# Kernel tuning notes

Measured on AMD Instinct MI355X. Metric: run time of the kernel, lower is better.

The kernel has to match this reference:

```python
import jax, jax.numpy as jnp
import numpy as np

S, B, C = 7, 2, 20
EPS = 1e-6
LAMBDA_COORD = 5.0
LAMBDA_NOOBJ = 0.5


def setup_inputs() -> dict:
    key = jax.random.key(0)
    k1, k2 = jax.random.split(key)
    N = 16384
    p = jax.random.uniform(k1, (N, S, S, B * 5 + C), dtype=jnp.float32)
    a = jax.random.uniform(k2, (N, S, S, B * 5 + C), dtype=jnp.float32)
    return {"p": p, "a": a}


def _attr(t, i):
    # i-th attribute of each of the B boxes: channels C+i, C+i+5, ... -> [N,S,S,B]
    return t[..., C + i::5]


def _coords(t):
    x, y, w, h = _attr(t, 0), _attr(t, 1), _attr(t, 2), _attr(t, 3)
    tl = jnp.stack((x - w / 2.0, y - h / 2.0), axis=-1)  # [N,S,S,B,2]
    br = jnp.stack((x + w / 2.0, y + h / 2.0), axis=-1)
    return tl, br


def _sse(x, y):
    return jnp.sum((x - y) ** 2)


def reference(p, a):
    # pairwise IoU between predicted boxes (axis 3) and target boxes (axis 4)
    p_tl, p_br = _coords(p)
    a_tl, a_br = _coords(a)
    tl = jnp.maximum(p_tl[:, :, :, :, None, :], a_tl[:, :, :, None, :, :])  # [N,S,S,B,B,2]
    br = jnp.minimum(p_br[:, :, :, :, None, :], a_br[:, :, :, None, :, :])
    sides = jnp.clip(br - tl, 0.0)
    inter = sides[..., 0] * sides[..., 1]  # [N,S,S,B,B]
    p_area = (_attr(p, 2) * _attr(p, 3))[:, :, :, :, None]
    a_area = (_attr(a, 2) * _attr(a, 3))[:, :, :, None, :]
    union = p_area + a_area - inter
    zero_union = union == 0.0
    iou = jnp.where(zero_union, 0.0, inter) / jnp.where(zero_union, EPS, union)
    max_iou = jnp.max(iou, axis=-1)  # [N,S,S,B]

    obj_i = (_attr(a, 4) > 0.0)[..., 0:1]  # [N,S,S,1]
    responsible = jnp.argmax(max_iou, axis=-1, keepdims=True) == jnp.arange(B)  # [N,S,S,B]
    obj_ij = (obj_i & responsible).astype(p.dtype)
    noobj_ij = 1.0 - obj_ij

    loss_x = _sse(obj_ij * _attr(a, 0), obj_ij * _attr(p, 0))
    loss_y = _sse(obj_ij * _attr(a, 1), obj_ij * _attr(p, 1))
    loss_w = _sse(obj_ij * jnp.sign(_attr(a, 2)) * jnp.sqrt(_attr(a, 2) + EPS),
                  obj_ij * jnp.sign(_attr(p, 2)) * jnp.sqrt(_attr(p, 2) + EPS))
    loss_h = _sse(obj_ij * jnp.sign(_attr(a, 3)) * jnp.sqrt(_attr(a, 3) + EPS),
                  obj_ij * jnp.sign(_attr(p, 3)) * jnp.sqrt(_attr(p, 3) + EPS))
    loss_conf_obj = _sse(obj_ij * obj_ij, obj_ij * _attr(p, 4))
    loss_conf_noobj = _sse(noobj_ij * obj_ij, noobj_ij * _attr(p, 4))
    obj_if = obj_i.astype(p.dtype)
    cls_loss = _sse(obj_if * p[..., 5 * B:], obj_if * a[..., 5 * B:])

    return (LAMBDA_COORD * (loss_x + loss_y + loss_w + loss_h)
            + loss_conf_obj + LAMBDA_NOOBJ * loss_conf_noobj + cls_loss)
```

## Files before the change

### kernel.cpp

```cpp
#include <hip/hip_runtime.h>


#define CH    30
#define EPSL  1e-6f
#define TPB   256

__device__ __forceinline__ float sgnf(float x) {
    return (x > 0.0f) ? 1.0f : ((x < 0.0f) ? -1.0f : 0.0f);
}

__global__ __launch_bounds__(TPB) void yolo_loss_kernel(const float* __restrict__ p,
                                                        const float* __restrict__ a,
                                                        float* __restrict__ out,
                                                        long long n_cells) {
    __shared__ float wsum[TPB / 64];

    const int tid = threadIdx.x;
    const long long cell = (long long)blockIdx.x * TPB + tid;

    float lsum = 0.0f;
    if (cell < n_cells) {
        const float2* cp2 = (const float2*)(p + cell * CH + 10);
        const float2* ca2 = (const float2*)(a + cell * CH + 10);
        float pd[20], ad[20];
#pragma unroll
        for (int i = 0; i < 10; ++i) {
            const float2 v = cp2[i];
            pd[2 * i] = v.x; pd[2 * i + 1] = v.y;
        }
#pragma unroll
        for (int i = 0; i < 10; ++i) {
            const float2 v = ca2[i];
            ad[2 * i] = v.x; ad[2 * i + 1] = v.y;
        }

        float pxv[2], pyv[2], pwv[2], phv[2], pcv[2];
        float axv[2], ayv[2], awv[2], ahv[2];
#pragma unroll
        for (int b = 0; b < 2; ++b) {
            pxv[b] = pd[10 + 5 * b]; pyv[b] = pd[11 + 5 * b];
            pwv[b] = pd[12 + 5 * b]; phv[b] = pd[13 + 5 * b];
            pcv[b] = pd[14 + 5 * b];
            axv[b] = ad[10 + 5 * b]; ayv[b] = ad[11 + 5 * b];
            awv[b] = ad[12 + 5 * b]; ahv[b] = ad[13 + 5 * b];
        }
        const bool obj = ad[14] > 0.0f;

        float miou[2];
#pragma unroll
        for (int pb = 0; pb < 2; ++pb) {
            const float p_tlx = pxv[pb] - 0.5f * pwv[pb];
            const float p_tly = pyv[pb] - 0.5f * phv[pb];
            const float p_brx = pxv[pb] + 0.5f * pwv[pb];
            const float p_bry = pyv[pb] + 0.5f * phv[pb];
            const float p_area = pwv[pb] * phv[pb];
            float best = -3.4e38f;
#pragma unroll
            for (int ab = 0; ab < 2; ++ab) {
                const float a_tlx = axv[ab] - 0.5f * awv[ab];
                const float a_tly = ayv[ab] - 0.5f * ahv[ab];
                const float a_brx = axv[ab] + 0.5f * awv[ab];
                const float a_bry = ayv[ab] + 0.5f * ahv[ab];
                float sx = fminf(p_brx, a_brx) - fmaxf(p_tlx, a_tlx);
                float sy = fminf(p_bry, a_bry) - fmaxf(p_tly, a_tly);
                sx = fmaxf(sx, 0.0f);
                sy = fmaxf(sy, 0.0f);
                const float inter = sx * sy;
                const float uni = p_area + awv[ab] * ahv[ab] - inter;
                const float iou = (uni == 0.0f) ? 0.0f : (inter / uni);
                best = fmaxf(best, iou);
            }
            miou[pb] = best;
        }
        const int resp = (miou[1] > miou[0]) ? 1 : 0;

#pragma unroll
        for (int b = 0; b < 2; ++b) {
            const bool oij = obj && (b == resp);
            if (oij) {
                const float dx = axv[b] - pxv[b];
                const float dy = ayv[b] - pyv[b];
                const float dw = sgnf(awv[b]) * sqrtf(awv[b] + EPSL) - sgnf(pwv[b]) * sqrtf(pwv[b] + EPSL);
                const float dh = sgnf(ahv[b]) * sqrtf(ahv[b] + EPSL) - sgnf(phv[b]) * sqrtf(phv[b] + EPSL);
                const float dc = 1.0f - pcv[b];
                lsum += 5.0f * (dx * dx + dy * dy + dw * dw + dh * dh) + dc * dc;
            } else {
                lsum += 0.5f * pcv[b] * pcv[b];
            }
        }

        if (obj) {
#pragma unroll
            for (int k = 0; k < 20; ++k) {
                const float d = pd[k] - ad[k];
                lsum += d * d;
            }
        }
    }

    float v = lsum;
#pragma unroll
    for (int off = 32; off > 0; off >>= 1)
        v += __shfl_down(v, off, 64);
    if ((tid & 63) == 0) wsum[tid >> 6] = v;
    __syncthreads();
    if (tid == 0) {
        float t = 0.0f;
#pragma unroll
        for (int w = 0; w < TPB / 64; ++w) t += wsum[w];
        atomicAdd(out, t);
    }
}

extern "C" void kernel_launch(void* const* d_in, const int* in_sizes, int n_in,
                              void* d_out, int out_size, void* d_ws, size_t ws_size,
                              hipStream_t stream) {
    const float* p = (const float*)d_in[0];
    const float* a = (const float*)d_in[1];
    float* out = (float*)d_out;

    const long long n_cells = (long long)in_sizes[0] / CH;
    const int grid = (int)((n_cells + TPB - 1) / TPB);

    hipMemsetAsync(d_out, 0, sizeof(float), stream);
    yolo_loss_kernel<<<grid, TPB, 0, stream>>>(p, a, out, n_cells);
}
```

Baseline: 204.0 us.

## Coalesce global loads via per-wave LDS transpose staging

Each wave now loads its 64 cells' relevant 20 floats cooperatively as float2 with lane-contiguous addresses, then transposes them through a padded shared-memory tile so each lane gets its own cell's data. This targets the strided per-thread 120-byte-stride loads of the old version, which gave poorly coalesced memory accesses. It adds LDS traffic and several block-wide barriers, and sets a minimum-occupancy launch bound that may constrain registers.

```diff
diff --git a/kernel.cpp b/kernel.cpp
--- a/kernel.cpp
+++ b/kernel.cpp
@@ -1,39 +1,82 @@
 #include <hip/hip_runtime.h>
 
 
-#define CH    30
-#define EPSL  1e-6f
-#define TPB   256
+#define CH       30
+#define EPSL     1e-6f
+#define TPB      256
+#define WAVES    (TPB / 64)
+#define CSTRIDE  22
+#define WTILE    (64 * CSTRIDE)
 
 __device__ __forceinline__ float sgnf(float x) {
     return (x > 0.0f) ? 1.0f : ((x < 0.0f) ? -1.0f : 0.0f);
 }
 
-__global__ __launch_bounds__(TPB) void yolo_loss_kernel(const float* __restrict__ p,
-                                                        const float* __restrict__ a,
-                                                        float* __restrict__ out,
-                                                        long long n_cells) {
-    __shared__ float wsum[TPB / 64];
+__global__ __launch_bounds__(TPB, 6) void yolo_loss_kernel(const float* __restrict__ p,
+                                                           const float* __restrict__ a,
+                                                           float* __restrict__ out,
+                                                           long long n_cells) {
+    __shared__ __align__(16) float sbuf[WAVES * WTILE];
+    __shared__ float wsum[WAVES];
 
-    const int tid = threadIdx.x;
-    const long long cell = (long long)blockIdx.x * TPB + tid;
+    const int tid  = threadIdx.x;
+    const int wave = tid >> 6;
+    const int lane = tid & 63;
+
+    const long long wave_cell0 = (long long)blockIdx.x * TPB + wave * 64;
+    int nc_wave = (int)min((long long)64, n_cells - wave_cell0);
+    if (nc_wave < 0) nc_wave = 0;
+
+    const char* pb = (const char*)p + wave_cell0 * 120LL;
+    const char* ab = (const char*)a + wave_cell0 * 120LL;
+    float* wbuf = &sbuf[wave * WTILE];
+
+    float2 rp[10], ra[10];
+    int cc[10], ss[10];
+#pragma unroll
+    for (int k = 0; k < 10; ++k) {
+        const int i = lane + 64 * k;
+        const int c = i / 10;
+        const int s = i - 10 * c;
+        cc[k] = c; ss[k] = s;
+        const int off = c * 120 + 40 + 8 * s;
+        if (c < nc_wave) rp[k] = *(const float2*)(pb + off);
+    }
+#pragma unroll
+    for (int k = 0; k < 10; ++k) {
+        const int off = cc[k] * 120 + 40 + 8 * ss[k];
+        if (cc[k] < nc_wave) ra[k] = *(const float2*)(ab + off);
+    }
+
+#pragma unroll
+    for (int k = 0; k < 10; ++k)
+        if (cc[k] < nc_wave)
+            *(float2*)&wbuf[cc[k] * CSTRIDE + 2 * ss[k]] = rp[k];
+    __syncthreads();
+
+    float pd[20];
+#pragma unroll
+    for (int s = 0; s < 10; ++s) {
+        const float2 v = *(const float2*)&wbuf[lane * CSTRIDE + 2 * s];
+        pd[2 * s] = v.x; pd[2 * s + 1] = v.y;
+    }
+    __syncthreads();
+
+#pragma unroll
+    for (int k = 0; k < 10; ++k)
+        if (cc[k] < nc_wave)
+            *(float2*)&wbuf[cc[k] * CSTRIDE + 2 * ss[k]] = ra[k];
+    __syncthreads();
+
+    float ad[20];
+#pragma unroll
+    for (int s = 0; s < 10; ++s) {
+        const float2 v = *(const float2*)&wbuf[lane * CSTRIDE + 2 * s];
+        ad[2 * s] = v.x; ad[2 * s + 1] = v.y;
+    }
 
     float lsum = 0.0f;
-    if (cell < n_cells) {
-        const float2* cp2 = (const float2*)(p + cell * CH + 10);
-        const float2* ca2 = (const float2*)(a + cell * CH + 10);
-        float pd[20], ad[20];
-#pragma unroll
-        for (int i = 0; i < 10; ++i) {
-            const float2 v = cp2[i];
-            pd[2 * i] = v.x; pd[2 * i + 1] = v.y;
-        }
-#pragma unroll
-        for (int i = 0; i < 10; ++i) {
-            const float2 v = ca2[i];
-            ad[2 * i] = v.x; ad[2 * i + 1] = v.y;
-        }
-
+    if (lane < nc_wave) {
         float pxv[2], pyv[2], pwv[2], phv[2], pcv[2];
         float axv[2], ayv[2], awv[2], ahv[2];
 #pragma unroll
@@ -48,29 +91,29 @@
 
         float miou[2];
 #pragma unroll
-        for (int pb = 0; pb < 2; ++pb) {
-            const float p_tlx = pxv[pb] - 0.5f * pwv[pb];
-            const float p_tly = pyv[pb] - 0.5f * phv[pb];
-            const float p_brx = pxv[pb] + 0.5f * pwv[pb];
-            const float p_bry = pyv[pb] + 0.5f * phv[pb];
-            const float p_area = pwv[pb] * phv[pb];
+        for (int pb2 = 0; pb2 < 2; ++pb2) {
+            const float p_tlx = pxv[pb2] - 0.5f * pwv[pb2];
+            const float p_tly = pyv[pb2] - 0.5f * phv[pb2];
+            const float p_brx = pxv[pb2] + 0.5f * pwv[pb2];
+            const float p_bry = pyv[pb2] + 0.5f * phv[pb2];
+            const float p_area = pwv[pb2] * phv[pb2];
             float best = -3.4e38f;
 #pragma unroll
-            for (int ab = 0; ab < 2; ++ab) {
-                const float a_tlx = axv[ab] - 0.5f * awv[ab];
-                const float a_tly = ayv[ab] - 0.5f * ahv[ab];
-                const float a_brx = axv[ab] + 0.5f * awv[ab];
-                const float a_bry = ayv[ab] + 0.5f * ahv[ab];
+            for (int ab2 = 0; ab2 < 2; ++ab2) {
+                const float a_tlx = axv[ab2] - 0.5f * awv[ab2];
+                const float a_tly = ayv[ab2] - 0.5f * ahv[ab2];
+                const float a_brx = axv[ab2] + 0.5f * awv[ab2];
+                const float a_bry = ayv[ab2] + 0.5f * ahv[ab2];
                 float sx = fminf(p_brx, a_brx) - fmaxf(p_tlx, a_tlx);
                 float sy = fminf(p_bry, a_bry) - fmaxf(p_tly, a_tly);
                 sx = fmaxf(sx, 0.0f);
                 sy = fmaxf(sy, 0.0f);
                 const float inter = sx * sy;
-                const float uni = p_area + awv[ab] * ahv[ab] - inter;
+                const float uni = p_area + awv[ab2] * ahv[ab2] - inter;
                 const float iou = (uni == 0.0f) ? 0.0f : (inter / uni);
                 best = fmaxf(best, iou);
             }
-            miou[pb] = best;
+            miou[pb2] = best;
         }
         const int resp = (miou[1] > miou[0]) ? 1 : 0;
 
@@ -102,12 +145,12 @@
 #pragma unroll
     for (int off = 32; off > 0; off >>= 1)
         v += __shfl_down(v, off, 64);
-    if ((tid & 63) == 0) wsum[tid >> 6] = v;
+    if (lane == 0) wsum[wave] = v;
     __syncthreads();
     if (tid == 0) {
         float t = 0.0f;
 #pragma unroll
-        for (int w = 0; w < TPB / 64; ++w) t += wsum[w];
+        for (int w = 0; w < WAVES; ++w) t += wsum[w];
         atomicAdd(out, t);
     }
 }
```

Measured after the change: 206.0 us. About the same (+1.0%).
